# Kernel tuning notes

Hardware: AMD Instinct MI355X
Metric: run time of the kernel (lower is better)

The kernel has to match this reference:

```python
import jax, jax.numpy as jnp
import numpy as np

N_U, N_M = 60000, 20000
F_U, F_M = 64, 128
IN_C, HID, OUT_C = 256, 256, 128
N = N_U + N_M
E = 500000
BN_EPS = 1e-5


def gcn_conv(z, W, b, src, dst, n):
    # PyG GCNConv: h = z @ W; add self-loops; symmetric norm D^-1/2 (A+I) D^-1/2; scatter-add; + bias
    h = z @ W                                        # [n, out]
    loop = jnp.arange(n)
    src_sl = jnp.concatenate([src, loop])            # [E+n]
    dst_sl = jnp.concatenate([dst, loop])
    deg = jax.ops.segment_sum(jnp.ones_like(dst_sl, h.dtype), dst_sl, num_segments=n)
    dinv = jax.lax.rsqrt(deg)                        # deg >= 1 due to self-loops
    norm = dinv[src_sl] * dinv[dst_sl]               # [E+n]
    msg = h[src_sl] * norm[:, None]                  # gather + scale
    out = jax.ops.segment_sum(msg, dst_sl, num_segments=n)
    return out + b


def batch_norm(z, gamma, beta):
    mean = jnp.mean(z, axis=0)
    var = jnp.var(z, axis=0)                         # biased, as torch BN uses for normalization
    return (z - mean) * jax.lax.rsqrt(var + BN_EPS) * gamma + beta


def setup_inputs() -> dict:
    key = jax.random.key(0)
    ks = jax.random.split(key, 13)
    x = jax.random.normal(ks[0], (N_U, F_U), jnp.float32)
    y = jax.random.normal(ks[1], (N_M, F_M), jnp.float32)
    edge_index = jax.random.randint(ks[2], (2, E), 0, N, dtype=jnp.int64)
    def lin(k, fin, fout):
        s = 1.0 / np.sqrt(fin)
        kw, kb = jax.random.split(k)
        return (jax.random.uniform(kw, (fin, fout), jnp.float32, -s, s),
                jax.random.uniform(kb, (fout,), jnp.float32, -s, s))
    fc1_w, fc1_b = lin(ks[3], F_U, IN_C)
    fc2_w, fc2_b = lin(ks[4], F_M, IN_C)
    conv1_w, conv1_b = lin(ks[5], IN_C, HID)
    conv2_w, conv2_b = lin(ks[6], HID, OUT_C)
    bn_gamma = jnp.ones((HID,), jnp.float32)
    bn_beta = jnp.zeros((HID,), jnp.float32)
    return {"x": x, "y": y, "edge_index": edge_index,
            "fc1_w": fc1_w, "fc1_b": fc1_b, "fc2_w": fc2_w, "fc2_b": fc2_b,
            "conv1_w": conv1_w, "conv1_b": conv1_b, "conv2_w": conv2_w, "conv2_b": conv2_b,
            "bn_gamma": bn_gamma, "bn_beta": bn_beta}


def reference(x, y, edge_index, fc1_w, fc1_b, fc2_w, fc2_b,
              conv1_w, conv1_b, conv2_w, conv2_b, bn_gamma, bn_beta):
    src, dst = edge_index[0], edge_index[1]
    xu = x @ fc1_w + fc1_b                           # [N_U, IN_C]
    xm = y @ fc2_w + fc2_b                           # [N_M, IN_C]
    z = jnp.concatenate([xu, xm], axis=0)            # [N, IN_C]
    z = gcn_conv(z, conv1_w, conv1_b, src, dst, N)   # [N, HID]
    z = jax.nn.relu(batch_norm(z, bn_gamma, bn_beta))
    z = gcn_conv(z, conv2_w, conv2_b, src, dst, N)   # [N, OUT_C]
    return z
```

## Files before the change

kernel.cpp:

```cpp
#include <hip/hip_runtime.h>
#include <math.h>
#include <stdint.h>

#define N_U 60000
#define N_M 20000
#define NN  80000
#define EE  500000
#define BN_EPS 1e-5f
#define NB_SCAN 313

typedef __attribute__((ext_vector_type(8))) short short8v;
typedef __attribute__((ext_vector_type(4))) float f32x4;

__device__ __forceinline__ unsigned short bf_hi(float f) {
    unsigned u = __float_as_uint(f);
    return (unsigned short)((u + 0x7FFFu + ((u >> 16) & 1u)) >> 16);
}
__device__ __forceinline__ float bf_f(unsigned short h) {
    return __uint_as_float(((unsigned)h) << 16);
}

__global__ void prep_kernel(const int* __restrict__ ei32, int* __restrict__ cnt,
                            int* __restrict__ cursor, int* __restrict__ rowptr,
                            float* __restrict__ sums, float* __restrict__ sumsq,
                            int* __restrict__ flag) {
    int i = blockIdx.x * blockDim.x + threadIdx.x;
    if (i < 256) { sums[i] = 0.f; sumsq[i] = 0.f; }
    for (int j = i; j < NN; j += gridDim.x * blockDim.x) { cnt[j] = 0; cursor[j] = 0; }
    if (i == 0) rowptr[NN] = EE;
    if (blockIdx.x == 0) {
        __shared__ int nz;
        if (threadIdx.x == 0) nz = 0;
        __syncthreads();
        int v = ei32[2 * threadIdx.x + 1];
        if (v != 0) atomicOr(&nz, 1);
        __syncthreads();
        if (threadIdx.x == 0) *flag = (nz == 0) ? 1 : 0;
    }
}

__device__ __forceinline__ int load_idx(const void* ei, int f, int pos) {
    return f ? (int)((const long long*)ei)[pos] : ((const int*)ei)[pos];
}

__global__ void hist_kernel(const void* __restrict__ ei, const int* __restrict__ flag,
                            int* __restrict__ cnt) {
    int f = *flag;
    int stride = gridDim.x * blockDim.x;
    for (int e = blockIdx.x * blockDim.x + threadIdx.x; e < EE; e += stride) {
        int d = load_idx(ei, f, EE + e);
        atomicAdd(&cnt[d], 1);
    }
}

__global__ void dinv_kernel(const int* __restrict__ cnt, float* __restrict__ dinv) {
    int i = blockIdx.x * blockDim.x + threadIdx.x;
    if (i < NN) dinv[i] = rsqrtf(1.0f + (float)cnt[i]);
}

__global__ void scan1_kernel(const int* __restrict__ cnt, int* __restrict__ rowptr,
                             int* __restrict__ blockSums) {
    __shared__ int sh[256];
    int tid = threadIdx.x;
    int i = blockIdx.x * 256 + tid;
    int v = (i < NN) ? cnt[i] : 0;
    int x = v;
    sh[tid] = x; __syncthreads();
#pragma unroll
    for (int off = 1; off < 256; off <<= 1) {
        int t = (tid >= off) ? sh[tid - off] : 0;
        __syncthreads();
        x += t; sh[tid] = x;
        __syncthreads();
    }
    if (i < NN) rowptr[i] = x - v;
    if (tid == 255) blockSums[blockIdx.x] = x;
}

__global__ void scan2_kernel(int* __restrict__ blockSums) {
    __shared__ int sh[512];
    int tid = threadIdx.x;
    int v = (tid < NB_SCAN) ? blockSums[tid] : 0;
    int x = v;
    sh[tid] = x; __syncthreads();
#pragma unroll
    for (int off = 1; off < 512; off <<= 1) {
        int t = (tid >= off) ? sh[tid - off] : 0;
        __syncthreads();
        x += t; sh[tid] = x;
        __syncthreads();
    }
    if (tid < NB_SCAN) blockSums[tid] = x - v;
}

__global__ void scan3_kernel(int* __restrict__ rowptr, const int* __restrict__ blockSums) {
    int i = blockIdx.x * 256 + threadIdx.x;
    if (i < NN) rowptr[i] += blockSums[blockIdx.x];
}

__global__ void fill_kernel(const void* __restrict__ ei, const int* __restrict__ flag,
                            const int* __restrict__ rowptr, int* __restrict__ cursor,
                            int* __restrict__ csr_src) {
    int f = *flag;
    int stride = gridDim.x * blockDim.x;
    for (int e = blockIdx.x * blockDim.x + threadIdx.x; e < EE; e += stride) {
        int s = load_idx(ei, f, e);
        int d = load_idx(ei, f, EE + e);
        int pos = rowptr[d] + atomicAdd(&cursor[d], 1);
        csr_src[pos] = s;
    }
}

__global__ void wsplit_kernel(const float* __restrict__ W1, const float* __restrict__ W2,
                              const float* __restrict__ Wf1, const float* __restrict__ Wf2,
                              short* __restrict__ W1tHi, short* __restrict__ W1tLo,
                              short* __restrict__ W2tHi, short* __restrict__ W2tLo,
                              short* __restrict__ Wf1tHi, short* __restrict__ Wf1tLo,
                              short* __restrict__ Wf2tHi, short* __restrict__ Wf2tLo) {
    int i = blockIdx.x * 256 + threadIdx.x;
    if (i < 256 * 256) {
        int k = i >> 8, n = i & 255;
        float v = W1[i];
        unsigned short h = bf_hi(v);
        unsigned short l = bf_hi(v - bf_f(h));
        W1tHi[n * 256 + k] = (short)h;
        W1tLo[n * 256 + k] = (short)l;
    }
    if (i < 256 * 128) {
        int k = i >> 7, n = i & 127;
        float v = W2[i];
        unsigned short h = bf_hi(v);
        unsigned short l = bf_hi(v - bf_f(h));
        W2tHi[n * 256 + k] = (short)h;
        W2tLo[n * 256 + k] = (short)l;
    }
    if (i < 64 * 256) {
        int k = i >> 8, n = i & 255;
        float v = Wf1[i];
        unsigned short h = bf_hi(v);
        unsigned short l = bf_hi(v - bf_f(h));
        Wf1tHi[n * 64 + k] = (short)h;
        Wf1tLo[n * 64 + k] = (short)l;
    }
    if (i < 128 * 256) {
        int k = i >> 8, n = i & 255;
        float v = Wf2[i];
        unsigned short h = bf_hi(v);
        unsigned short l = bf_hi(v - bf_f(h));
        Wf2tHi[n * 128 + k] = (short)h;
        Wf2tLo[n * 128 + k] = (short)l;
    }
}

template <int K, int N, int MODE, bool BNRELU, bool OUTBF16>
__global__ __launch_bounds__(256) void mfma_gemm_kernel(
    int M, const float* __restrict__ A, const short* __restrict__ WtHi,
    const short* __restrict__ WtLo, const float* __restrict__ ep,
    const float* __restrict__ bnsc, const float* __restrict__ bnsh,
    float* __restrict__ Out, short* __restrict__ OutB) {
    constexpr int LDT = 40;
    __shared__ short AsHi[128 * LDT];
    __shared__ short AsLo[128 * LDT];
    __shared__ short BsHi[128 * LDT];
    __shared__ short BsLo[128 * LDT];
    const int tid  = threadIdx.x;
    const int lane = tid & 63, wave = tid >> 6;
    const int wm = (wave >> 1) * 64, wn = (wave & 1) * 64;
    const int R0 = blockIdx.x * 128;
    const int n0 = blockIdx.y * 128;
    const int srow  = tid >> 1;
    const int shalf = (tid & 1) * 16;
    const int l15  = lane & 15;
    const int koff = (lane >> 4) * 8;

    f32x4 acc[4][4];
#pragma unroll
    for (int mi = 0; mi < 4; ++mi)
#pragma unroll
        for (int ni = 0; ni < 4; ++ni)
            acc[mi][ni] = (f32x4){0.f, 0.f, 0.f, 0.f};

    const int arow = min(R0 + srow, M - 1);

    for (int k0 = 0; k0 < K; k0 += 32) {
        const float4* ga = (const float4*)&A[(size_t)arow * K + k0 + shalf];
        float4 a0 = ga[0], a1 = ga[1], a2 = ga[2], a3 = ga[3];
        const int4* gwh = (const int4*)&WtHi[(size_t)(n0 + srow) * K + k0 + shalf];
        const int4* gwl = (const int4*)&WtLo[(size_t)(n0 + srow) * K + k0 + shalf];
        int4 wh0 = gwh[0], wh1 = gwh[1];
        int4 wl0 = gwl[0], wl1 = gwl[1];

        if (BNRELU) {
            const float4* gs = (const float4*)&bnsc[k0 + shalf];
            const float4* gh = (const float4*)&bnsh[k0 + shalf];
            float4 s0 = gs[0], s1 = gs[1], s2 = gs[2], s3 = gs[3];
            float4 t0 = gh[0], t1 = gh[1], t2 = gh[2], t3 = gh[3];
#define BNR4(a, s, t)                                                          \
            a.x = fmaxf(a.x * s.x + t.x, 0.f);                                 \
            a.y = fmaxf(a.y * s.y + t.y, 0.f);                                 \
            a.z = fmaxf(a.z * s.z + t.z, 0.f);                                 \
            a.w = fmaxf(a.w * s.w + t.w, 0.f);
            BNR4(a0, s0, t0); BNR4(a1, s1, t1); BNR4(a2, s2, t2); BNR4(a3, s3, t3);
#undef BNR4
        }

        unsigned h[8], l[8];
#define SPLIT4(v, hA, hB, lA, lB)                                              \
        {                                                                      \
            unsigned short h0_ = bf_hi(v.x), h1_ = bf_hi(v.y);                 \
            unsigned short h2_ = bf_hi(v.z), h3_ = bf_hi(v.w);                 \
            unsigned short l0_ = bf_hi(v.x - bf_f(h0_));                       \
            unsigned short l1_ = bf_hi(v.y - bf_f(h1_));                       \
            unsigned short l2_ = bf_hi(v.z - bf_f(h2_));                       \
            unsigned short l3_ = bf_hi(v.w - bf_f(h3_));                       \
            hA = (unsigned)h0_ | ((unsigned)h1_ << 16);                        \
            hB = (unsigned)h2_ | ((unsigned)h3_ << 16);                        \
            lA = (unsigned)l0_ | ((unsigned)l1_ << 16);                        \
            lB = (unsigned)l2_ | ((unsigned)l3_ << 16);                        \
        }
        SPLIT4(a0, h[0], h[1], l[0], l[1]);
        SPLIT4(a1, h[2], h[3], l[2], l[3]);
        SPLIT4(a2, h[4], h[5], l[4], l[5]);
        SPLIT4(a3, h[6], h[7], l[6], l[7]);
#undef SPLIT4

        __syncthreads();
        int4* dAH = (int4*)&AsHi[srow * LDT + shalf];
        int4* dAL = (int4*)&AsLo[srow * LDT + shalf];
        dAH[0] = make_int4((int)h[0], (int)h[1], (int)h[2], (int)h[3]);
        dAH[1] = make_int4((int)h[4], (int)h[5], (int)h[6], (int)h[7]);
        dAL[0] = make_int4((int)l[0], (int)l[1], (int)l[2], (int)l[3]);
        dAL[1] = make_int4((int)l[4], (int)l[5], (int)l[6], (int)l[7]);
        int4* dBH = (int4*)&BsHi[srow * LDT + shalf];
        int4* dBL = (int4*)&BsLo[srow * LDT + shalf];
        dBH[0] = wh0; dBH[1] = wh1;
        dBL[0] = wl0; dBL[1] = wl1;
        __syncthreads();

        short8v bh[4], bl[4];
#pragma unroll
        for (int ni = 0; ni < 4; ++ni) {
            int nrow = wn + ni * 16 + l15;
            bh[ni] = *(const short8v*)&BsHi[nrow * LDT + koff];
            bl[ni] = *(const short8v*)&BsLo[nrow * LDT + koff];
        }
#pragma unroll
        for (int mi = 0; mi < 4; ++mi) {
            int mrow = wm + mi * 16 + l15;
            short8v ah = *(const short8v*)&AsHi[mrow * LDT + koff];
            short8v al = *(const short8v*)&AsLo[mrow * LDT + koff];
#pragma unroll
            for (int ni = 0; ni < 4; ++ni) {
                acc[mi][ni] = __builtin_amdgcn_mfma_f32_16x16x32_bf16(ah, bh[ni], acc[mi][ni], 0, 0, 0);
                acc[mi][ni] = __builtin_amdgcn_mfma_f32_16x16x32_bf16(ah, bl[ni], acc[mi][ni], 0, 0, 0);
                acc[mi][ni] = __builtin_amdgcn_mfma_f32_16x16x32_bf16(al, bh[ni], acc[mi][ni], 0, 0, 0);
            }
        }
    }

#pragma unroll
    for (int mi = 0; mi < 4; ++mi) {
#pragma unroll
        for (int i = 0; i < 4; ++i) {
            int row = R0 + wm + mi * 16 + (lane >> 4) * 4 + i;
            if (row < M) {
                float sc = (MODE == 0) ? ep[row] : 1.0f;
#pragma unroll
                for (int ni = 0; ni < 4; ++ni) {
                    int col = n0 + wn + ni * 16 + l15;
                    float v = acc[mi][ni][i];
                    v = (MODE == 0) ? v * sc : v + ep[col];
                    if (OUTBF16)
                        OutB[(size_t)row * N + col] = (short)bf_hi(v);
                    else
                        Out[(size_t)row * N + col] = v;
                }
            }
        }
    }
}

__device__ __forceinline__ void acc_bf4(float4& a, ushort4 v) {
    a.x += bf_f(v.x); a.y += bf_f(v.y); a.z += bf_f(v.z); a.w += bf_f(v.w);
}

__global__ __launch_bounds__(256) void gather256_kernel(const short* __restrict__ h,
                                                        const float* __restrict__ bias,
                                                        const float* __restrict__ dinv,
                                                        const int* __restrict__ rowptr,
                                                        const int* __restrict__ csr_src,
                                                        float* __restrict__ out) {
    int wid = threadIdx.x >> 6, lane = threadIdx.x & 63;
    int r = blockIdx.x * 4 + wid;
    if (r >= NN) return;
    int beg = rowptr[r], end = rowptr[r + 1];
    float dr = dinv[r];
    const ushort4* hp = (const ushort4*)h;
    float4 acc = {0.f, 0.f, 0.f, 0.f};
    acc_bf4(acc, hp[(size_t)r * 64 + lane]);
    int k = beg;
    for (; k + 3 < end; k += 4) {
        int s0 = csr_src[k], s1 = csr_src[k + 1], s2 = csr_src[k + 2], s3 = csr_src[k + 3];
        ushort4 v0 = hp[(size_t)s0 * 64 + lane];
        ushort4 v1 = hp[(size_t)s1 * 64 + lane];
        ushort4 v2 = hp[(size_t)s2 * 64 + lane];
        ushort4 v3 = hp[(size_t)s3 * 64 + lane];
        acc_bf4(acc, v0); acc_bf4(acc, v1); acc_bf4(acc, v2); acc_bf4(acc, v3);
    }
    for (; k < end; ++k)
        acc_bf4(acc, hp[(size_t)csr_src[k] * 64 + lane]);
    float4 b = ((const float4*)bias)[lane];
    float4 o;
    o.x = b.x + dr * acc.x; o.y = b.y + dr * acc.y;
    o.z = b.z + dr * acc.z; o.w = b.w + dr * acc.w;
    ((float4*)(out + (size_t)r * 256))[lane] = o;
}

__global__ __launch_bounds__(256) void gather128_kernel(const short* __restrict__ h,
                                                        const float* __restrict__ bias,
                                                        const float* __restrict__ dinv,
                                                        const int* __restrict__ rowptr,
                                                        const int* __restrict__ csr_src,
                                                        float* __restrict__ out) {
    int sub = threadIdx.x >> 5, lane = threadIdx.x & 31;
    int r = blockIdx.x * 8 + sub;
    if (r >= NN) return;
    int beg = rowptr[r], end = rowptr[r + 1];
    float dr = dinv[r];
    const ushort4* hp = (const ushort4*)h;
    float4 acc = {0.f, 0.f, 0.f, 0.f};
    acc_bf4(acc, hp[(size_t)r * 32 + lane]);
    int k = beg;
    for (; k + 3 < end; k += 4) {
        int s0 = csr_src[k], s1 = csr_src[k + 1], s2 = csr_src[k + 2], s3 = csr_src[k + 3];
        ushort4 v0 = hp[(size_t)s0 * 32 + lane];
        ushort4 v1 = hp[(size_t)s1 * 32 + lane];
        ushort4 v2 = hp[(size_t)s2 * 32 + lane];
        ushort4 v3 = hp[(size_t)s3 * 32 + lane];
        acc_bf4(acc, v0); acc_bf4(acc, v1); acc_bf4(acc, v2); acc_bf4(acc, v3);
    }
    for (; k < end; ++k)
        acc_bf4(acc, hp[(size_t)csr_src[k] * 32 + lane]);
    float4 b = ((const float4*)bias)[lane];
    float4 o;
    o.x = b.x + dr * acc.x; o.y = b.y + dr * acc.y;
    o.z = b.z + dr * acc.z; o.w = b.w + dr * acc.w;
    ((float4*)(out + (size_t)r * 128))[lane] = o;
}

__global__ __launch_bounds__(256) void bn_stats_kernel(const float* __restrict__ a,
                                                       float* __restrict__ sums,
                                                       float* __restrict__ sumsq) {
    __shared__ float shs[256], shs2[256];
    int tid = threadIdx.x;
    int wid = tid >> 6, lane = tid & 63;
    shs[tid] = 0.f; shs2[tid] = 0.f;
    __syncthreads();
    float4 s = {0.f, 0.f, 0.f, 0.f}, s2 = {0.f, 0.f, 0.f, 0.f};
    for (int row = blockIdx.x * 4 + wid; row < NN; row += gridDim.x * 4) {
        float4 v = ((const float4*)(a + (size_t)row * 256))[lane];
        s.x += v.x; s.y += v.y; s.z += v.z; s.w += v.w;
        s2.x += v.x * v.x; s2.y += v.y * v.y; s2.z += v.z * v.z; s2.w += v.w * v.w;
    }
    atomicAdd(&shs[4 * lane + 0], s.x);  atomicAdd(&shs2[4 * lane + 0], s2.x);
    atomicAdd(&shs[4 * lane + 1], s.y);  atomicAdd(&shs2[4 * lane + 1], s2.y);
    atomicAdd(&shs[4 * lane + 2], s.z);  atomicAdd(&shs2[4 * lane + 2], s2.z);
    atomicAdd(&shs[4 * lane + 3], s.w);  atomicAdd(&shs2[4 * lane + 3], s2.w);
    __syncthreads();
    atomicAdd(&sums[tid], shs[tid]);
    atomicAdd(&sumsq[tid], shs2[tid]);
}

__global__ void bn_final_kernel(const float* __restrict__ sums, const float* __restrict__ sumsq,
                                const float* __restrict__ gamma, const float* __restrict__ beta,
                                float* __restrict__ scale, float* __restrict__ shift) {
    int c = threadIdx.x;
    const float Nf = (float)NN;
    float mean = sums[c] / Nf;
    float var = sumsq[c] / Nf - mean * mean;
    float sc = gamma[c] * rsqrtf(var + BN_EPS);
    scale[c] = sc;
    shift[c] = beta[c] - mean * sc;
}

extern "C" void kernel_launch(void* const* d_in, const int* in_sizes, int n_in,
                              void* d_out, int out_size, void* d_ws, size_t ws_size,
                              hipStream_t stream) {
    const float* x       = (const float*)d_in[0];
    const float* y       = (const float*)d_in[1];
    const void*  ei      = d_in[2];
    const float* fc1_w   = (const float*)d_in[3];
    const float* fc1_b   = (const float*)d_in[4];
    const float* fc2_w   = (const float*)d_in[5];
    const float* fc2_b   = (const float*)d_in[6];
    const float* conv1_w = (const float*)d_in[7];
    const float* conv1_b = (const float*)d_in[8];
    const float* conv2_w = (const float*)d_in[9];
    const float* conv2_b = (const float*)d_in[10];
    const float* gamma   = (const float*)d_in[11];
    const float* beta    = (const float*)d_in[12];
    float* out = (float*)d_out;

    float* ws = (float*)d_ws;
    float* bufA = ws;
    float* bufB = ws + (size_t)NN * 256;
    float* aux  = bufB + (size_t)NN * 256;
    float* dinv  = aux;
    float* sums  = dinv + NN;
    float* sumsq = sums + 256;
    float* scale = sumsq + 256;
    float* shift = scale + 256;
    int*   flag      = (int*)(shift + 256);
    int*   cnt       = flag + 1;
    int*   rowptr    = cnt + NN;
    int*   cursor    = rowptr + NN + 1;
    int*   blockSums = cursor + NN;
    int*   csr_src   = blockSums + NB_SCAN + 3;
    short* w1th = (short*)(((uintptr_t)(csr_src + EE) + 15) & ~(uintptr_t)15);
    short* w1tl = w1th + 256 * 256;
    short* w2th = w1tl + 256 * 256;
    short* w2tl = w2th + 256 * 128;
    short* wf1h = w2tl + 256 * 128;
    short* wf1l = wf1h + 256 * 64;
    short* wf2h = wf1l + 256 * 64;
    short* wf2l = wf2h + 256 * 128;
    short* hB   = (short*)bufB;

    prep_kernel<<<320, 256, 0, stream>>>((const int*)ei, cnt, cursor, rowptr, sums, sumsq, flag);
    hist_kernel<<<1024, 256, 0, stream>>>(ei, flag, cnt);
    dinv_kernel<<<(NN + 255) / 256, 256, 0, stream>>>(cnt, dinv);
    scan1_kernel<<<NB_SCAN, 256, 0, stream>>>(cnt, rowptr, blockSums);
    scan2_kernel<<<1, 512, 0, stream>>>(blockSums);
    scan3_kernel<<<NB_SCAN, 256, 0, stream>>>(rowptr, blockSums);
    fill_kernel<<<1024, 256, 0, stream>>>(ei, flag, rowptr, cursor, csr_src);
    wsplit_kernel<<<256, 256, 0, stream>>>(conv1_w, conv2_w, fc1_w, fc2_w,
                                           w1th, w1tl, w2th, w2tl, wf1h, wf1l, wf2h, wf2l);

    mfma_gemm_kernel<64, 256, 1, false, false><<<dim3(469, 2), 256, 0, stream>>>(
        N_U, x, wf1h, wf1l, fc1_b, nullptr, nullptr, bufA, nullptr);
    mfma_gemm_kernel<128, 256, 1, false, false><<<dim3(157, 2), 256, 0, stream>>>(
        N_M, y, wf2h, wf2l, fc2_b, nullptr, nullptr, bufA + (size_t)N_U * 256, nullptr);

    mfma_gemm_kernel<256, 256, 0, false, true><<<dim3(625, 2), 256, 0, stream>>>(
        NN, bufA, w1th, w1tl, dinv, nullptr, nullptr, nullptr, hB);
    gather256_kernel<<<NN / 4, 256, 0, stream>>>(hB, conv1_b, dinv, rowptr, csr_src, bufA);

    bn_stats_kernel<<<256, 256, 0, stream>>>(bufA, sums, sumsq);
    bn_final_kernel<<<1, 256, 0, stream>>>(sums, sumsq, gamma, beta, scale, shift);

    mfma_gemm_kernel<256, 128, 0, true, true><<<dim3(625, 1), 256, 0, stream>>>(
        NN, bufA, w2th, w2tl, dinv, scale, shift, nullptr, hB);
    gather128_kernel<<<NN / 8, 256, 0, stream>>>(hB, conv2_b, dinv, rowptr, csr_src, out);
}
```

Baseline: 402.5 us.

## Pre-swizzle weights into MFMA fragment layout and load B directly from global

```diff
diff --git a/kernel.cpp b/kernel.cpp
--- a/kernel.cpp
+++ b/kernel.cpp
@@ -111,58 +111,31 @@
     }
 }
 
-__global__ void wsplit_kernel(const float* __restrict__ W1, const float* __restrict__ W2,
-                              const float* __restrict__ Wf1, const float* __restrict__ Wf2,
-                              short* __restrict__ W1tHi, short* __restrict__ W1tLo,
-                              short* __restrict__ W2tHi, short* __restrict__ W2tLo,
-                              short* __restrict__ Wf1tHi, short* __restrict__ Wf1tLo,
-                              short* __restrict__ Wf2tHi, short* __restrict__ Wf2tLo) {
+template <int K, int N>
+__global__ void wsplit_frag_kernel(const float* __restrict__ W,
+                                   short* __restrict__ Hi, short* __restrict__ Lo) {
     int i = blockIdx.x * 256 + threadIdx.x;
-    if (i < 256 * 256) {
-        int k = i >> 8, n = i & 255;
-        float v = W1[i];
-        unsigned short h = bf_hi(v);
-        unsigned short l = bf_hi(v - bf_f(h));
-        W1tHi[n * 256 + k] = (short)h;
-        W1tLo[n * 256 + k] = (short)l;
-    }
-    if (i < 256 * 128) {
-        int k = i >> 7, n = i & 127;
-        float v = W2[i];
-        unsigned short h = bf_hi(v);
-        unsigned short l = bf_hi(v - bf_f(h));
-        W2tHi[n * 256 + k] = (short)h;
-        W2tLo[n * 256 + k] = (short)l;
-    }
-    if (i < 64 * 256) {
-        int k = i >> 8, n = i & 255;
-        float v = Wf1[i];
-        unsigned short h = bf_hi(v);
-        unsigned short l = bf_hi(v - bf_f(h));
-        Wf1tHi[n * 64 + k] = (short)h;
-        Wf1tLo[n * 64 + k] = (short)l;
-    }
-    if (i < 128 * 256) {
-        int k = i >> 8, n = i & 255;
-        float v = Wf2[i];
-        unsigned short h = bf_hi(v);
-        unsigned short l = bf_hi(v - bf_f(h));
-        Wf2tHi[n * 128 + k] = (short)h;
-        Wf2tLo[n * 128 + k] = (short)l;
-    }
+    if (i >= K * N) return;
+    int k = i / N, n = i - k * N;
+    float v = W[i];
+    unsigned short h = bf_hi(v);
+    unsigned short l = bf_hi(v - bf_f(h));
+    int nt = n >> 4, r = n & 15, kt = k >> 5, q = (k >> 3) & 3, p = k & 7;
+    int idx = ((nt * (K / 32) + kt) << 9) + (q << 7) + (r << 3) + p;
+    Hi[idx] = (short)h;
+    Lo[idx] = (short)l;
 }
 
 template <int K, int N, int MODE, bool BNRELU, bool OUTBF16>
 __global__ __launch_bounds__(256) void mfma_gemm_kernel(
-    int M, const float* __restrict__ A, const short* __restrict__ WtHi,
-    const short* __restrict__ WtLo, const float* __restrict__ ep,
+    int M, const float* __restrict__ A, const short* __restrict__ WfHi,
+    const short* __restrict__ WfLo, const float* __restrict__ ep,
     const float* __restrict__ bnsc, const float* __restrict__ bnsh,
     float* __restrict__ Out, short* __restrict__ OutB) {
     constexpr int LDT = 40;
+    constexpr int NT = K / 32;
     __shared__ short AsHi[128 * LDT];
     __shared__ short AsLo[128 * LDT];
-    __shared__ short BsHi[128 * LDT];
-    __shared__ short BsLo[128 * LDT];
     const int tid  = threadIdx.x;
     const int lane = tid & 63, wave = tid >> 6;
     const int wm = (wave >> 1) * 64, wn = (wave & 1) * 64;
@@ -172,6 +145,7 @@
     const int shalf = (tid & 1) * 16;
     const int l15  = lane & 15;
     const int koff = (lane >> 4) * 8;
+    const int nt0  = (n0 + wn) >> 4;
 
     f32x4 acc[4][4];
 #pragma unroll
@@ -181,14 +155,16 @@
             acc[mi][ni] = (f32x4){0.f, 0.f, 0.f, 0.f};
 
     const int arow = min(R0 + srow, M - 1);
-
-    for (int k0 = 0; k0 < K; k0 += 32) {
-        const float4* ga = (const float4*)&A[(size_t)arow * K + k0 + shalf];
-        float4 a0 = ga[0], a1 = ga[1], a2 = ga[2], a3 = ga[3];
-        const int4* gwh = (const int4*)&WtHi[(size_t)(n0 + srow) * K + k0 + shalf];
-        const int4* gwl = (const int4*)&WtLo[(size_t)(n0 + srow) * K + k0 + shalf];
-        int4 wh0 = gwh[0], wh1 = gwh[1];
-        int4 wl0 = gwl[0], wl1 = gwl[1];
+    const float* abase = &A[(size_t)arow * K + shalf];
+
+    float4 a0 = ((const float4*)abase)[0];
+    float4 a1 = ((const float4*)abase)[1];
+    float4 a2 = ((const float4*)abase)[2];
+    float4 a3 = ((const float4*)abase)[3];
+
+#pragma unroll
+    for (int kt = 0; kt < NT; ++kt) {
+        const int k0 = kt * 32;
 
         if (BNRELU) {
             const float4* gs = (const float4*)&bnsc[k0 + shalf];
@@ -231,19 +207,21 @@
         dAH[1] = make_int4((int)h[4], (int)h[5], (int)h[6], (int)h[7]);
         dAL[0] = make_int4((int)l[0], (int)l[1], (int)l[2], (int)l[3]);
         dAL[1] = make_int4((int)l[4], (int)l[5], (int)l[6], (int)l[7]);
-        int4* dBH = (int4*)&BsHi[srow * LDT + shalf];
-        int4* dBL = (int4*)&BsLo[srow * LDT + shalf];
-        dBH[0] = wh0; dBH[1] = wh1;
-        dBL[0] = wl0; dBL[1] = wl1;
-        __syncthreads();
+        __syncthreads();
+
+        if (kt + 1 < NT) {
+            const float4* gnext = (const float4*)(abase + (kt + 1) * 32);
+            a0 = gnext[0]; a1 = gnext[1]; a2 = gnext[2]; a3 = gnext[3];
+        }
 
         short8v bh[4], bl[4];
 #pragma unroll
         for (int ni = 0; ni < 4; ++ni) {
-            int nrow = wn + ni * 16 + l15;
-            bh[ni] = *(const short8v*)&BsHi[nrow * LDT + koff];
-            bl[ni] = *(const short8v*)&BsLo[nrow * LDT + koff];
-        }
+            int fidx = (((nt0 + ni) * NT + kt) << 9) + lane * 8;
+            bh[ni] = *(const short8v*)&WfHi[fidx];
+            bl[ni] = *(const short8v*)&WfLo[fidx];
+        }
+
 #pragma unroll
         for (int mi = 0; mi < 4; ++mi) {
             int mrow = wm + mi * 16 + l15;
@@ -433,8 +411,10 @@
     scan2_kernel<<<1, 512, 0, stream>>>(blockSums);
     scan3_kernel<<<NB_SCAN, 256, 0, stream>>>(rowptr, blockSums);
     fill_kernel<<<1024, 256, 0, stream>>>(ei, flag, rowptr, cursor, csr_src);
-    wsplit_kernel<<<256, 256, 0, stream>>>(conv1_w, conv2_w, fc1_w, fc2_w,
-                                           w1th, w1tl, w2th, w2tl, wf1h, wf1l, wf2h, wf2l);
+    wsplit_frag_kernel<256, 256><<<256, 256, 0, stream>>>(conv1_w, w1th, w1tl);
+    wsplit_frag_kernel<256, 128><<<128, 256, 0, stream>>>(conv2_w, w2th, w2tl);
+    wsplit_frag_kernel<64, 256><<<64, 256, 0, stream>>>(fc1_w, wf1h, wf1l);
+    wsplit_frag_kernel<128, 256><<<128, 256, 0, stream>>>(fc2_w, wf2h, wf2l);
 
     mfma_gemm_kernel<64, 256, 1, false, false><<<dim3(469, 2), 256, 0, stream>>>(
         N_U, x, wf1h, wf1l, fc1_b, nullptr, nullptr, bufA, nullptr);
```

Result: no change. 398.8 us (-0.9%).
